# Optimization experiments

Measured on AMD Instinct MI355X. Metric: run time of the kernel, lower is better.

Reference implementation:

```python
import math
import jax, jax.numpy as jnp
import numpy as np

PI_APPROX = 3.1415926  # the module's hard-coded pi in KVal


def _factratio(N, D):
    # python-float replica of PRT.factratio
    if N >= D:
        p = 1.0
        for i in range(D + 1, N + 1):
            p *= i
        return p
    p = 1.0
    for i in range(N + 1, D + 1):
        p *= i
    return 1.0 / p


def _kval(M, L):
    return math.sqrt((2 * L + 1) / (4 * PI_APPROX) * _factratio(L - M, L + M))


def _assoc_legendre(M, L, x):
    # x = cos(theta), |x| <= 1 by construction so the zero-guard branch never fires
    pmm = jnp.ones_like(x)
    if M > 0:
        somx2 = jnp.sqrt((1.0 + x) * (1.0 - x))
        fact = 1.0
        for _ in range(1, M + 1):
            pmm = -pmm * fact * somx2
            fact = fact + 2
    if L == M:
        return pmm
    pmmp1 = x * (2 * M + 1) * pmm
    if L == M + 1:
        return pmmp1
    pll = pmmp1
    for i in range(M + 2, L + 1):
        pll = (x * (2 * i - 1) * pmmp1 - (i + M - 1) * pmm) / (i - M)
        pmm, pmmp1 = pmmp1, pll
    return pll


def _spherical_harmonic(M, L, theta, phi):
    sqrt2 = math.sqrt(2.0)
    ct = jnp.cos(theta)
    if M > 0:
        return sqrt2 * _kval(M, L) * jnp.cos(M * phi) * _assoc_legendre(M, L, ct)
    elif M < 0:
        return sqrt2 * _kval(-M, L) * jnp.sin(-M * phi) * _assoc_legendre(-M, L, ct)
    else:
        return _kval(0, L) * _assoc_legendre(0, L, ct)


def _sh_coeffs(order, phi, theta):
    # [N_rays, S, (order+1)^2] -- loop is over the small fixed harmonic index set
    shs = [_spherical_harmonic(m, l, theta, phi)
           for l in range(order + 1) for m in range(-l, l + 1)]
    return jnp.stack(shs, axis=-1)


def setup_inputs() -> dict:
    key = jax.random.key(0)
    k1, k2, k3 = jax.random.split(key, 3)
    N_RAYS, N, ORDER = 32768, 16, 3
    S = N * N
    xv = jax.random.uniform(k1, (N_RAYS, S), dtype=jnp.float32)
    yv = jax.random.uniform(k2, (N_RAYS, S), dtype=jnp.float32)
    theta = jnp.arccos(1.0 - 2.0 * xv)          # matches sampleSphericalDirections_N_rays
    phi = (2.0 * math.pi) * yv
    # binary visibility per sphere sample
    p_vis = (jax.random.uniform(k3, (N_RAYS, S, 1), dtype=jnp.float32) > 0.5).astype(jnp.float32)
    return {"p_vis": p_vis, "phi": phi, "theta": theta, "n": N, "order": ORDER}


def reference(p_vis, phi, theta, n, order):
    sh = _sh_coeffs(order, phi, theta)           # [R, S, K]
    w = 4.0 * math.pi / (n * n)                   # module uses math.pi here
    prt = jnp.sum(sh * p_vis, axis=1)             # [R, K]
    return jnp.clip(prt * w, -2.0, 2.0)
```

## Files before the change

kernel.cpp:

```cpp
#include <hip/hip_runtime.h>
#include <math.h>


static __device__ __forceinline__ float clampf(float v) {
    return fminf(fmaxf(v, -2.0f), 2.0f);
}

__global__ __launch_bounds__(256) void prt_kernel(
    const float* __restrict__ vis,
    const float* __restrict__ phi,
    const float* __restrict__ theta,
    const int* __restrict__ n_ptr,
    float* __restrict__ out,
    int n_rays)
{
    const int lane = threadIdx.x & 63;
    const int wave = threadIdx.x >> 6;
    const int ray  = blockIdx.x * 4 + wave;
    if (ray >= n_rays) return;

    const int base = ray * 256 + lane * 4;

    const float4 ph = *reinterpret_cast<const float4*>(phi + base);
    const float4 th = *reinterpret_cast<const float4*>(theta + base);
    const float4 vv = *reinterpret_cast<const float4*>(vis + base);

    const float* phs = reinterpret_cast<const float*>(&ph);
    const float* ths = reinterpret_cast<const float*>(&th);
    const float* vvs = reinterpret_cast<const float*>(&vv);

    float acc[16];
    #pragma unroll
    for (int i = 0; i < 16; ++i) acc[i] = 0.0f;

    #pragma unroll
    for (int j = 0; j < 4; ++j) {
        const float x  = __cosf(ths[j]);
        const float sq = (1.0f + x) * (1.0f - x);
        const float s  = __fsqrt_rn(sq);
        float sp, cp;
        __sincosf(phs[j], &sp, &cp);
        const float s2 = 2.0f * sp * cp;
        const float c2 = 1.0f - 2.0f * sp * sp;
        const float s3 = s2 * cp + c2 * sp;
        const float c3 = c2 * cp - s2 * sp;

        const float v    = vvs[j];
        const float vx   = v * x;
        const float vx2  = vx * x;
        const float vx3  = vx2 * x;
        const float vsq  = v * sq;
        const float vxsq = vx * sq;
        const float vsqs = vsq * s;
        const float t1   = v * s;
        const float t2   = vx * s;
        const float t3   = vx2 * s;

        acc[0]  += v;
        acc[1]  += t1 * sp;
        acc[2]  += vx;
        acc[3]  += t1 * cp;
        acc[4]  += vsq * s2;
        acc[5]  += t2 * sp;
        acc[6]  += vx2;
        acc[7]  += t2 * cp;
        acc[8]  += vsq * c2;
        acc[9]  += vsqs * s3;
        acc[10] += vxsq * s2;
        acc[11] += t3 * sp;
        acc[12] += vx3;
        acc[13] += t3 * cp;
        acc[14] += vxsq * c2;
        acc[15] += vsqs * c3;
    }

    #pragma unroll
    for (int m = 1; m < 64; m <<= 1) {
        #pragma unroll
        for (int i = 0; i < 16; ++i)
            acc[i] += __shfl_xor(acc[i], m, 64);
    }

    if (lane == 0) {
        const int n = *n_ptr;
        const float w = 12.566370614359172f / (float)(n * n);

        const float K00 =  0.28209479f;
        const float K10 =  0.48860251f;
        const float A1  = -0.48860251f;
        const float A2  =  0.54627422f;
        const float B1  = -1.09254843f;
        const float K20 =  0.63078314f;
        const float A3  = -0.59004360f;
        const float B2  =  1.44530570f;
        const float C1  = -0.45704579f;
        const float K30 =  0.74635267f;

        float o[16];
        o[0]  = K00 * acc[0];
        o[1]  = A1  * acc[1];
        o[2]  = K10 * acc[2];
        o[3]  = A1  * acc[3];
        o[4]  = A2  * acc[4];
        o[5]  = B1  * acc[5];
        o[6]  = K20 * (1.5f * acc[6] - 0.5f * acc[0]);
        o[7]  = B1  * acc[7];
        o[8]  = A2  * acc[8];
        o[9]  = A3  * acc[9];
        o[10] = B2  * acc[10];
        o[11] = C1  * (5.0f * acc[11] - acc[1]);
        o[12] = K30 * (2.5f * acc[12] - 1.5f * acc[2]);
        o[13] = C1  * (5.0f * acc[13] - acc[3]);
        o[14] = B2  * acc[14];
        o[15] = A3  * acc[15];

        float4* op = reinterpret_cast<float4*>(out + ray * 16);
        #pragma unroll
        for (int q = 0; q < 4; ++q) {
            float4 t;
            t.x = clampf(o[q * 4 + 0] * w);
            t.y = clampf(o[q * 4 + 1] * w);
            t.z = clampf(o[q * 4 + 2] * w);
            t.w = clampf(o[q * 4 + 3] * w);
            op[q] = t;
        }
    }
}

extern "C" void kernel_launch(void* const* d_in, const int* in_sizes, int n_in,
                              void* d_out, int out_size, void* d_ws, size_t ws_size,
                              hipStream_t stream) {
    const float* vis   = (const float*)d_in[0];
    const float* phi   = (const float*)d_in[1];
    const float* theta = (const float*)d_in[2];
    const int*   n_ptr = (const int*)d_in[3];

    float* out = (float*)d_out;

    const int n_rays = in_sizes[1] / 256;
    const int blocks = (n_rays + 3) / 4;
    prt_kernel<<<blocks, 256, 0, stream>>>(vis, phi, theta, n_ptr, out, n_rays);
}
```

Measured before the change: 134.4 us.

## Use transpose-style butterfly reduction and fold Legendre terms into per-sample accumulation

Replaces the full 16x6 xor-shuffle all-reduce with a recursive-halving butterfly. Each step lets lanes swap half of their accumulators, so the shuffle count drops from 96 to about 19, and each of the first 16 lanes ends up owning one coefficient. The Legendre combinations are now formed per sample, and theta is handled with a single sincos instead of cos plus sqrt. Output scaling and clamping are spread across 16 lanes with per-lane constant selection, replacing the serial lane-0 epilogue. The risk is extra select instructions and small numerical differences from computing sin(theta) directly.

```diff
diff --git a/kernel.cpp b/kernel.cpp
--- a/kernel.cpp
+++ b/kernel.cpp
@@ -1,10 +1,6 @@
 #include <hip/hip_runtime.h>
 #include <math.h>
 
-
-static __device__ __forceinline__ float clampf(float v) {
-    return fminf(fmaxf(v, -2.0f), 2.0f);
-}
 
 __global__ __launch_bounds__(256) void prt_kernel(
     const float* __restrict__ vis,
@@ -35,96 +31,107 @@
 
     #pragma unroll
     for (int j = 0; j < 4; ++j) {
-        const float x  = __cosf(ths[j]);
-        const float sq = (1.0f + x) * (1.0f - x);
-        const float s  = __fsqrt_rn(sq);
+        float s, x;
+        __sincosf(ths[j], &s, &x);
         float sp, cp;
         __sincosf(phs[j], &sp, &cp);
+
+        const float sq = s * s;
         const float s2 = 2.0f * sp * cp;
-        const float c2 = 1.0f - 2.0f * sp * sp;
-        const float s3 = s2 * cp + c2 * sp;
-        const float c3 = c2 * cp - s2 * sp;
+        const float c2 = fmaf(-2.0f * sp, sp, 1.0f);
+        const float s3 = fmaf(s2, cp, c2 * sp);
+        const float c3 = fmaf(-s2, sp, c2 * cp);
 
         const float v    = vvs[j];
+        const float t1   = v * s;
         const float vx   = v * x;
-        const float vx2  = vx * x;
-        const float vx3  = vx2 * x;
+        const float t2   = vx * s;
         const float vsq  = v * sq;
         const float vxsq = vx * sq;
         const float vsqs = vsq * s;
-        const float t1   = v * s;
-        const float t2   = vx * s;
-        const float t3   = vx2 * s;
+
+        const float x2  = x * x;
+        const float P20 = fmaf(1.5f, x2, -0.5f);
+        const float q1  = fmaf(5.0f, x2, -1.0f);
+        const float r30 = fmaf(2.5f, x2, -1.5f);
+        const float t1q = t1 * q1;
 
         acc[0]  += v;
-        acc[1]  += t1 * sp;
+        acc[1]   = fmaf(t1,   sp,  acc[1]);
         acc[2]  += vx;
-        acc[3]  += t1 * cp;
-        acc[4]  += vsq * s2;
-        acc[5]  += t2 * sp;
-        acc[6]  += vx2;
-        acc[7]  += t2 * cp;
-        acc[8]  += vsq * c2;
-        acc[9]  += vsqs * s3;
-        acc[10] += vxsq * s2;
-        acc[11] += t3 * sp;
-        acc[12] += vx3;
-        acc[13] += t3 * cp;
-        acc[14] += vxsq * c2;
-        acc[15] += vsqs * c3;
+        acc[3]   = fmaf(t1,   cp,  acc[3]);
+        acc[4]   = fmaf(vsq,  s2,  acc[4]);
+        acc[5]   = fmaf(t2,   sp,  acc[5]);
+        acc[6]   = fmaf(v,    P20, acc[6]);
+        acc[7]   = fmaf(t2,   cp,  acc[7]);
+        acc[8]   = fmaf(vsq,  c2,  acc[8]);
+        acc[9]   = fmaf(vsqs, s3,  acc[9]);
+        acc[10]  = fmaf(vxsq, s2,  acc[10]);
+        acc[11]  = fmaf(t1q,  sp,  acc[11]);
+        acc[12]  = fmaf(vx,   r30, acc[12]);
+        acc[13]  = fmaf(t1q,  cp,  acc[13]);
+        acc[14]  = fmaf(vxsq, c2,  acc[14]);
+        acc[15]  = fmaf(vsqs, c3,  acc[15]);
     }
 
+    const bool b0 = (lane & 1) != 0;
+    const bool b1 = (lane & 2) != 0;
+    const bool b2 = (lane & 4) != 0;
+    const bool b3 = (lane & 8) != 0;
+
     #pragma unroll
-    for (int m = 1; m < 64; m <<= 1) {
-        #pragma unroll
-        for (int i = 0; i < 16; ++i)
-            acc[i] += __shfl_xor(acc[i], m, 64);
+    for (int j = 0; j < 8; ++j) {
+        const float a0 = acc[2 * j], a1 = acc[2 * j + 1];
+        const float keep = b0 ? a1 : a0;
+        const float give = b0 ? a0 : a1;
+        acc[j] = keep + __shfl_xor(give, 1, 64);
     }
+    #pragma unroll
+    for (int j = 0; j < 4; ++j) {
+        const float a0 = acc[2 * j], a1 = acc[2 * j + 1];
+        const float keep = b1 ? a1 : a0;
+        const float give = b1 ? a0 : a1;
+        acc[j] = keep + __shfl_xor(give, 2, 64);
+    }
+    #pragma unroll
+    for (int j = 0; j < 2; ++j) {
+        const float a0 = acc[2 * j], a1 = acc[2 * j + 1];
+        const float keep = b2 ? a1 : a0;
+        const float give = b2 ? a0 : a1;
+        acc[j] = keep + __shfl_xor(give, 4, 64);
+    }
+    float r;
+    {
+        const float keep = b3 ? acc[1] : acc[0];
+        const float give = b3 ? acc[0] : acc[1];
+        r = keep + __shfl_xor(give, 8, 64);
+    }
+    r += __shfl_xor(r, 16, 64);
+    r += __shfl_xor(r, 32, 64);
 
-    if (lane == 0) {
-        const int n = *n_ptr;
-        const float w = 12.566370614359172f / (float)(n * n);
+    const float k01   = b0 ? -0.48860253f : 0.28209481f;
+    const float k23   = b0 ? -0.48860253f : 0.48860253f;
+    const float k45   = b0 ? -1.09254847f : 0.54627424f;
+    const float k67   = b0 ? -1.09254847f : 0.63078316f;
+    const float k89   = b0 ? -0.59004360f : 0.54627424f;
+    const float k1011 = b0 ? -0.45704580f : 1.44530571f;
+    const float k1213 = b0 ? -0.45704580f : 0.74635269f;
+    const float k1415 = b0 ? -0.59004360f : 1.44530571f;
+    const float ka = b1 ? k23 : k01;
+    const float kb = b1 ? k67 : k45;
+    const float kc = b1 ? k1011 : k89;
+    const float kd = b1 ? k1415 : k1213;
+    const float ke = b2 ? kb : ka;
+    const float kf = b2 ? kd : kc;
+    const float K  = b3 ? kf : ke;
 
-        const float K00 =  0.28209479f;
-        const float K10 =  0.48860251f;
-        const float A1  = -0.48860251f;
-        const float A2  =  0.54627422f;
-        const float B1  = -1.09254843f;
-        const float K20 =  0.63078314f;
-        const float A3  = -0.59004360f;
-        const float B2  =  1.44530570f;
-        const float C1  = -0.45704579f;
-        const float K30 =  0.74635267f;
+    const int n = *n_ptr;
+    const float w = 12.566370614359172f / (float)(n * n);
 
-        float o[16];
-        o[0]  = K00 * acc[0];
-        o[1]  = A1  * acc[1];
-        o[2]  = K10 * acc[2];
-        o[3]  = A1  * acc[3];
-        o[4]  = A2  * acc[4];
-        o[5]  = B1  * acc[5];
-        o[6]  = K20 * (1.5f * acc[6] - 0.5f * acc[0]);
-        o[7]  = B1  * acc[7];
-        o[8]  = A2  * acc[8];
-        o[9]  = A3  * acc[9];
-        o[10] = B2  * acc[10];
-        o[11] = C1  * (5.0f * acc[11] - acc[1]);
-        o[12] = K30 * (2.5f * acc[12] - 1.5f * acc[2]);
-        o[13] = C1  * (5.0f * acc[13] - acc[3]);
-        o[14] = B2  * acc[14];
-        o[15] = A3  * acc[15];
+    const float res = fminf(fmaxf(r * K * w, -2.0f), 2.0f);
 
-        float4* op = reinterpret_cast<float4*>(out + ray * 16);
-        #pragma unroll
-        for (int q = 0; q < 4; ++q) {
-            float4 t;
-            t.x = clampf(o[q * 4 + 0] * w);
-            t.y = clampf(o[q * 4 + 1] * w);
-            t.z = clampf(o[q * 4 + 2] * w);
-            t.w = clampf(o[q * 4 + 3] * w);
-            op[q] = t;
-        }
-    }
+    if (lane < 16)
+        out[ray * 16 + lane] = res;
 }
 
 extern "C" void kernel_launch(void* const* d_in, const int* in_sizes, int n_in,
```

Result: faster. 119.9 us (-10.8%).
